# Kernel optimization log

Hardware: AMD Instinct MI355X
Metric: run time of the kernel (lower is better)

The kernel has to match this reference:

```python
import math
import jax, jax.numpy as jnp
import numpy as np

FACTOR = 5


def setup_inputs() -> dict:
    key = jax.random.key(0)
    kq, kk, kv, ki = jax.random.split(key, 4)
    B, H, L, D = 4, 8, 2048, 64
    sample_k = min(FACTOR * math.ceil(math.log(L)), L)  # 40
    queries = jax.random.normal(kq, (B, H, L, D), dtype=jnp.float32)
    keys = jax.random.normal(kk, (B, H, L, D), dtype=jnp.float32)
    values = jax.random.normal(kv, (B, H, L, D), dtype=jnp.float32)
    index_sample = jax.random.randint(ki, (L, sample_k), 0, L, dtype=jnp.int64 if jax.config.jax_enable_x64 else jnp.int32)
    return {"queries": queries, "keys": keys, "values": values, "index_sample": index_sample}


def reference(queries, keys, values, index_sample):
    B, H, L_Q, D = queries.shape
    L_K = keys.shape[2]
    u = min(FACTOR * math.ceil(math.log(L_Q)), L_Q)  # n_top queries (= 40)
    scale = 1.0 / math.sqrt(D)

    # --- _prob_QK: sparsity measurement over randomly sampled keys ---
    # K_sample[b,h,q,s,:] = keys[b,h,index_sample[q,s],:]  -> [B,H,L_Q,S,D]
    K_sample = keys[:, :, index_sample, :]
    Q_K_sample = jnp.einsum('bhqd,bhqsd->bhqs', queries, K_sample)  # [B,H,L_Q,S]
    M = Q_K_sample.max(axis=-1) - Q_K_sample.sum(axis=-1) / L_K      # [B,H,L_Q]
    _, M_top = jax.lax.top_k(M, u)                                    # [B,H,u]

    Q_reduce = jnp.take_along_axis(queries, M_top[..., None], axis=2)  # [B,H,u,D]
    scores_top = jnp.einsum('bhud,bhkd->bhuk', Q_reduce, keys) * scale  # [B,H,u,L_K]

    # --- initial context: causal cumulative sum of V (mask_flag=True) ---
    context = jnp.cumsum(values, axis=2)  # [B,H,L_Q,D]

    # --- ProbMask: causal rows gathered at the selected query indices ---
    causal = jnp.triu(jnp.ones((L_Q, L_K), dtype=bool), 1)  # [L_Q,L_K]
    mask = causal[M_top]                                     # [B,H,u,L_K]
    scores_top = jnp.where(mask, -jnp.inf, scores_top)

    attn = jax.nn.softmax(scores_top, axis=-1)                       # [B,H,u,L_K]
    update = jnp.einsum('bhuk,bhkd->bhud', attn, values)             # [B,H,u,D]

    b_idx = jnp.arange(B)[:, None, None]
    h_idx = jnp.arange(H)[None, :, None]
    context = context.at[b_idx, h_idx, M_top].set(update.astype(context.dtype))
    return context
```

## Files before the change

kernel.cpp:

```cpp
#include <hip/hip_runtime.h>
#include <math.h>

#define BB 4
#define HH 8
#define LL 2048
#define DD 64
#define SK 40
#define BH (BB*HH)
#define TILE 256
#define NTILE (LL/TILE)

__device__ __forceinline__ unsigned ordu(float v) {
    unsigned u = __float_as_uint(v);
    return (u & 0x80000000u) ? ~u : (u | 0x80000000u);
}

__global__ __launch_bounds__(256) void compute_M_kernel(
        const float* __restrict__ Q, const float* __restrict__ K,
        const int* __restrict__ IDX, float* __restrict__ M) {
    int x = blockIdx.x;
    int bhLo = x & 7;
    int r = x >> 3;
    int bhHi = r & 3;
    int chunk = r >> 2;
    int bh = bhHi * 8 + bhLo;
    int qbase = chunk * 64;
    int tid = threadIdx.x;
    int w = tid >> 6, lane = tid & 63;
    int qw = lane >> 2, c = lane & 3;
    int qi = w * 16 + qw;
    int qpos = qbase + qi;

    __shared__ int sidx[64 * SK];
    for (int i = tid; i < 64 * SK; i += 256) sidx[i] = IDX[(size_t)qbase * SK + i];

    const float4* Q4 = (const float4*)Q;
    const float4* K4 = (const float4*)K;
    float4 qreg[4];
    #pragma unroll
    for (int j = 0; j < 4; ++j)
        qreg[j] = Q4[((size_t)bh * LL + qpos) * 16 + j * 4 + c];
    __syncthreads();

    size_t kb4 = (size_t)bh * LL * 16;
    float mx = -INFINITY, sm = 0.f;
    #pragma unroll 8
    for (int s = 0; s < SK; ++s) {
        int ks = sidx[qi * SK + s];
        const float4* kr = K4 + kb4 + (size_t)ks * 16;
        float p = 0.f;
        #pragma unroll
        for (int j = 0; j < 4; ++j) {
            float4 kv = kr[j * 4 + c];
            p += qreg[j].x * kv.x + qreg[j].y * kv.y + qreg[j].z * kv.z + qreg[j].w * kv.w;
        }
        p += __shfl_xor(p, 1, 64);
        p += __shfl_xor(p, 2, 64);
        mx = fmaxf(mx, p);
        sm += p;
    }
    if (c == 0) M[(size_t)bh * LL + qpos] = mx - sm * (1.0f / (float)LL);
}

__global__ __launch_bounds__(1024) void topk_kernel(const float* __restrict__ M,
                                                    int* __restrict__ topk) {
    int bh = blockIdx.x;
    int tid = threadIdx.x;
    __shared__ unsigned hist[256];
    __shared__ unsigned bc_prefix, bc_need;
    __shared__ unsigned cnt_gt, cnt_eq;
    __shared__ int eqlist[128];

    unsigned v0 = ordu(M[(size_t)bh * LL + tid]);
    unsigned v1 = ordu(M[(size_t)bh * LL + tid + 1024]);

    unsigned prefix = 0, need = SK;
    #pragma unroll
    for (int pass = 0; pass < 4; ++pass) {
        const int s = 24 - 8 * pass;
        const unsigned maskHigh = (pass == 0) ? 0u : (0xFFFFFFFFu << (s + 8));
        if (tid < 256) hist[tid] = 0;
        __syncthreads();
        if (((v0 ^ prefix) & maskHigh) == 0) atomicAdd(&hist[(v0 >> s) & 0xFF], 1u);
        if (((v1 ^ prefix) & maskHigh) == 0) atomicAdd(&hist[(v1 >> s) & 0xFF], 1u);
        __syncthreads();
        if (tid < 256) {
            unsigned above = 0;
            for (int b = tid + 1; b < 256; ++b) above += hist[b];
            if (above < need && above + hist[tid] >= need) {
                bc_prefix = prefix | ((unsigned)tid << s);
                bc_need = need - above;
            }
        }
        __syncthreads();
        prefix = bc_prefix;
        need = bc_need;
        __syncthreads();
    }
    unsigned T = prefix;
    if (tid == 0) { cnt_gt = 0; cnt_eq = 0; }
    __syncthreads();
    if (v0 > T) { unsigned p = atomicAdd(&cnt_gt, 1u); topk[bh * SK + p] = tid; }
    else if (v0 == T) { unsigned p = atomicAdd(&cnt_eq, 1u); if (p < 128) eqlist[p] = tid; }
    if (v1 > T) { unsigned p = atomicAdd(&cnt_gt, 1u); topk[bh * SK + p] = tid + 1024; }
    else if (v1 == T) { unsigned p = atomicAdd(&cnt_eq, 1u); if (p < 128) eqlist[p] = tid + 1024; }
    __syncthreads();
    if (tid == 0) {
        int ne = (int)min(cnt_eq, 128u);
        unsigned base = cnt_gt;
        for (unsigned r2 = 0; r2 < need; ++r2) {
            int bj = 0, bv = 0x7FFFFFFF;
            for (int j = 0; j < ne; ++j)
                if (eqlist[j] < bv) { bv = eqlist[j]; bj = j; }
            topk[bh * SK + base + r2] = bv;
            eqlist[bj] = 0x7FFFFFFF;
        }
    }
}

__global__ __launch_bounds__(256) void vsum_kernel(const float* __restrict__ V,
                                                   float* __restrict__ csum) {
    int x = blockIdx.x;
    int bhLo = x & 7, r = x >> 3;
    int bhHi = r & 3, c = r >> 2;
    int bh = bhHi * 8 + bhLo;
    int tid = threadIdx.x;
    int d = tid & 63, sg = tid >> 6;
    size_t base = (size_t)bh * LL * DD;
    int row0 = c * 128 + sg * 32;
    float s = 0.f;
    for (int j = 0; j < 32; ++j) s += V[base + (size_t)(row0 + j) * DD + d];
    __shared__ float part[4][DD];
    part[sg][d] = s;
    __syncthreads();
    if (sg == 0)
        csum[((size_t)bh * 16 + c) * DD + d] = part[0][d] + part[1][d] + part[2][d] + part[3][d];
}

__global__ __launch_bounds__(256) void cumsum_kernel(const float* __restrict__ V,
                                                     const float* __restrict__ csum,
                                                     float* __restrict__ out) {
    int x = blockIdx.x;
    int bhLo = x & 7, r = x >> 3;
    int bhHi = r & 3, c = r >> 2;
    int bh = bhHi * 8 + bhLo;
    int tid = threadIdx.x;
    int d = tid & 63, sg = tid >> 6;
    size_t base = (size_t)bh * LL * DD;
    int row0 = c * 128 + sg * 32;
    float v[32];
    #pragma unroll
    for (int j = 0; j < 32; ++j) v[j] = V[base + (size_t)(row0 + j) * DD + d];
    float s = 0.f;
    #pragma unroll
    for (int j = 0; j < 32; ++j) s += v[j];
    __shared__ float part[4][DD];
    part[sg][d] = s;
    __syncthreads();
    float pre = 0.f;
    for (int cc = 0; cc < c; ++cc) pre += csum[((size_t)bh * 16 + cc) * DD + d];
    for (int ss = 0; ss < sg; ++ss) pre += part[ss][d];
    float acc = pre;
    #pragma unroll
    for (int j = 0; j < 32; ++j) {
        acc += v[j];
        out[base + (size_t)(row0 + j) * DD + d] = acc;
    }
}

__global__ __launch_bounds__(256) void attn_part_kernel(
        const float* __restrict__ Q, const float* __restrict__ K,
        const float* __restrict__ V, const int* __restrict__ topk,
        float* __restrict__ ml, float* __restrict__ ov) {
    int x = blockIdx.x;
    int bhLo = x & 7;
    int r = x >> 3;
    int u = r % SK;
    int y = r / SK;
    int bhHi = y & 3;
    int tile = y >> 2;
    int bh = bhHi * 8 + bhLo;
    int tid = threadIdx.x;

    int qpos = topk[bh * SK + u];
    int kstart = tile * TILE;
    if (kstart > qpos) return;
    int nk = min(TILE, qpos + 1 - kstart);

    const float4* Q4 = (const float4*)Q;
    const float4* K4 = (const float4*)K;
    const float4* V4 = (const float4*)V;

    int w = tid >> 6, lane = tid & 63;
    int kw = lane >> 2, c = lane & 3;
    float4 qreg[4];
    #pragma unroll
    for (int j = 0; j < 4; ++j)
        qreg[j] = Q4[((size_t)bh * LL + qpos) * 16 + j * 4 + c];

    __shared__ float se[TILE];
    __shared__ float red[4], red2[4];
    __shared__ float opart[16][16][4];

    size_t kb4 = ((size_t)bh * LL + kstart) * 16;
    #pragma unroll
    for (int rr = 0; rr < 4; ++rr) {
        int key = w * 64 + rr * 16 + kw;
        const float4* kr = K4 + kb4 + (size_t)key * 16;
        float p = 0.f;
        #pragma unroll
        for (int j = 0; j < 4; ++j) {
            float4 kv = kr[j * 4 + c];
            p += qreg[j].x * kv.x + qreg[j].y * kv.y + qreg[j].z * kv.z + qreg[j].w * kv.w;
        }
        p += __shfl_xor(p, 1, 64);
        p += __shfl_xor(p, 2, 64);
        if (c == 0) se[key] = (key < nk) ? p * 0.125f : -INFINITY;
    }
    __syncthreads();

    float sc = se[tid];
    float wv = sc;
    #pragma unroll
    for (int off = 32; off > 0; off >>= 1) wv = fmaxf(wv, __shfl_xor(wv, off, 64));
    if (lane == 0) red[w] = wv;
    __syncthreads();
    float m = fmaxf(fmaxf(red[0], red[1]), fmaxf(red[2], red[3]));
    float e = expf(sc - m);
    se[tid] = e;
    float ws = e;
    #pragma unroll
    for (int off = 32; off > 0; off >>= 1) ws += __shfl_xor(ws, off, 64);
    if (lane == 0) red2[w] = ws;
    __syncthreads();

    int slot = (bh * SK + u) * NTILE + tile;
    if (tid == 0) {
        ml[(size_t)slot * 2]     = m;
        ml[(size_t)slot * 2 + 1] = red2[0] + red2[1] + red2[2] + red2[3];
    }

    int col4 = tid & 15, kg = tid >> 4;
    float ax = 0.f, ay = 0.f, az = 0.f, aw = 0.f;
    #pragma unroll 4
    for (int j = kg; j < nk; j += 16) {
        float sj = se[j];
        float4 vv = V4[((size_t)bh * LL + kstart + j) * 16 + col4];
        ax += sj * vv.x; ay += sj * vv.y; az += sj * vv.z; aw += sj * vv.w;
    }
    opart[kg][col4][0] = ax;
    opart[kg][col4][1] = ay;
    opart[kg][col4][2] = az;
    opart[kg][col4][3] = aw;
    __syncthreads();
    if (tid < DD) {
        int c4 = tid >> 2, cp = tid & 3;
        float s = 0.f;
        #pragma unroll
        for (int kg2 = 0; kg2 < 16; ++kg2) s += opart[kg2][c4][cp];
        ov[(size_t)slot * DD + tid] = s;
    }
}

__global__ __launch_bounds__(64) void attn_combine_kernel(
        const int* __restrict__ topk, const float* __restrict__ ml,
        const float* __restrict__ ov, float* __restrict__ out) {
    int bh = blockIdx.x / SK;
    int u  = blockIdx.x % SK;
    int d = threadIdx.x;
    int qpos = topk[bh * SK + u];
    int ntile = (qpos >> 8) + 1;
    int slot0 = (bh * SK + u) * NTILE;
    float gm = -INFINITY;
    for (int t = 0; t < ntile; ++t) gm = fmaxf(gm, ml[(size_t)(slot0 + t) * 2]);
    float o = 0.f, l = 0.f;
    for (int t = 0; t < ntile; ++t) {
        float wgt = expf(ml[(size_t)(slot0 + t) * 2] - gm);
        l += ml[(size_t)(slot0 + t) * 2 + 1] * wgt;
        o += ov[(size_t)(slot0 + t) * DD + d] * wgt;
    }
    out[(size_t)bh * LL * DD + (size_t)qpos * DD + d] = o / l;
}

extern "C" void kernel_launch(void* const* d_in, const int* in_sizes, int n_in,
                              void* d_out, int out_size, void* d_ws, size_t ws_size,
                              hipStream_t stream) {
    const float* Q   = (const float*)d_in[0];
    const float* K   = (const float*)d_in[1];
    const float* V   = (const float*)d_in[2];
    const int*   IDX = (const int*)d_in[3];
    float* out = (float*)d_out;

    char* ws = (char*)d_ws;
    float* M    = (float*)ws;  ws += (size_t)BH * LL * sizeof(float);
    int*   topk = (int*)ws;    ws += ((size_t)BH * SK * sizeof(int) + 255) & ~255ull;
    float* csum = (float*)ws;  ws += (size_t)BH * 16 * DD * sizeof(float);
    float* ml   = (float*)ws;  ws += (size_t)BH * SK * NTILE * 2 * sizeof(float);
    float* ov   = (float*)ws;

    compute_M_kernel<<<1024, 256, 0, stream>>>(Q, K, IDX, M);
    topk_kernel<<<BH, 1024, 0, stream>>>(M, topk);
    vsum_kernel<<<512, 256, 0, stream>>>(V, csum);
    cumsum_kernel<<<512, 256, 0, stream>>>(V, csum, out);
    attn_part_kernel<<<BH * SK * NTILE, 256, 0, stream>>>(Q, K, V, topk, ml, ov);
    attn_combine_kernel<<<BH * SK, 64, 0, stream>>>(topk, ml, ov, out);
}
```

Before: 167.8 us.

## Merge six launches into three and drop split-K attention combine

Folds the M computation and the V chunk-sum into one launch, and the cumsum and top-k selection into another (top-k now uses 256 threads with 8 values each). The attention step now processes the whole causal key range per selected query in a single block, using a 2048-entry shared score buffer, so the partial/combine kernels and their workspace go away. This removes launch overhead and intermediate traffic, but each attention block now walks up to 2048 keys serially, which can leave the GPU underfilled with only 1280 blocks of uneven length.

```diff
diff --git a/kernel.cpp b/kernel.cpp
--- a/kernel.cpp
+++ b/kernel.cpp
@@ -7,185 +7,181 @@
 #define DD 64
 #define SK 40
 #define BH (BB*HH)
-#define TILE 256
-#define NTILE (LL/TILE)
 
 __device__ __forceinline__ unsigned ordu(float v) {
     unsigned u = __float_as_uint(v);
     return (u & 0x80000000u) ? ~u : (u | 0x80000000u);
 }
 
-__global__ __launch_bounds__(256) void compute_M_kernel(
+__global__ __launch_bounds__(256) void stage1_kernel(
         const float* __restrict__ Q, const float* __restrict__ K,
-        const int* __restrict__ IDX, float* __restrict__ M) {
-    int x = blockIdx.x;
-    int bhLo = x & 7;
-    int r = x >> 3;
-    int bhHi = r & 3;
-    int chunk = r >> 2;
-    int bh = bhHi * 8 + bhLo;
-    int qbase = chunk * 64;
+        const float* __restrict__ V, const int* __restrict__ IDX,
+        float* __restrict__ M, float* __restrict__ csum) {
     int tid = threadIdx.x;
-    int w = tid >> 6, lane = tid & 63;
-    int qw = lane >> 2, c = lane & 3;
-    int qi = w * 16 + qw;
-    int qpos = qbase + qi;
-
-    __shared__ int sidx[64 * SK];
-    for (int i = tid; i < 64 * SK; i += 256) sidx[i] = IDX[(size_t)qbase * SK + i];
-
-    const float4* Q4 = (const float4*)Q;
-    const float4* K4 = (const float4*)K;
-    float4 qreg[4];
-    #pragma unroll
-    for (int j = 0; j < 4; ++j)
-        qreg[j] = Q4[((size_t)bh * LL + qpos) * 16 + j * 4 + c];
-    __syncthreads();
-
-    size_t kb4 = (size_t)bh * LL * 16;
-    float mx = -INFINITY, sm = 0.f;
-    #pragma unroll 8
-    for (int s = 0; s < SK; ++s) {
-        int ks = sidx[qi * SK + s];
-        const float4* kr = K4 + kb4 + (size_t)ks * 16;
-        float p = 0.f;
-        #pragma unroll
-        for (int j = 0; j < 4; ++j) {
-            float4 kv = kr[j * 4 + c];
-            p += qreg[j].x * kv.x + qreg[j].y * kv.y + qreg[j].z * kv.z + qreg[j].w * kv.w;
-        }
-        p += __shfl_xor(p, 1, 64);
-        p += __shfl_xor(p, 2, 64);
-        mx = fmaxf(mx, p);
-        sm += p;
-    }
-    if (c == 0) M[(size_t)bh * LL + qpos] = mx - sm * (1.0f / (float)LL);
-}
-
-__global__ __launch_bounds__(1024) void topk_kernel(const float* __restrict__ M,
-                                                    int* __restrict__ topk) {
-    int bh = blockIdx.x;
+    if (blockIdx.x < 1024) {
+        int x = blockIdx.x;
+        int bhLo = x & 7;
+        int r = x >> 3;
+        int bhHi = r & 3;
+        int chunk = r >> 2;
+        int bh = bhHi * 8 + bhLo;
+        int qbase = chunk * 64;
+        int w = tid >> 6, lane = tid & 63;
+        int qw = lane >> 2, c = lane & 3;
+        int qi = w * 16 + qw;
+        int qpos = qbase + qi;
+
+        __shared__ int sidx[64 * SK];
+        for (int i = tid; i < 64 * SK; i += 256) sidx[i] = IDX[(size_t)qbase * SK + i];
+
+        const float4* Q4 = (const float4*)Q;
+        const float4* K4 = (const float4*)K;
+        float4 qreg[4];
+        #pragma unroll
+        for (int j = 0; j < 4; ++j)
+            qreg[j] = Q4[((size_t)bh * LL + qpos) * 16 + j * 4 + c];
+        __syncthreads();
+
+        size_t kb4 = (size_t)bh * LL * 16;
+        float mx = -INFINITY, sm = 0.f;
+        #pragma unroll 8
+        for (int s = 0; s < SK; ++s) {
+            int ks = sidx[qi * SK + s];
+            const float4* kr = K4 + kb4 + (size_t)ks * 16;
+            float p = 0.f;
+            #pragma unroll
+            for (int j = 0; j < 4; ++j) {
+                float4 kv = kr[j * 4 + c];
+                p += qreg[j].x * kv.x + qreg[j].y * kv.y + qreg[j].z * kv.z + qreg[j].w * kv.w;
+            }
+            p += __shfl_xor(p, 1, 64);
+            p += __shfl_xor(p, 2, 64);
+            mx = fmaxf(mx, p);
+            sm += p;
+        }
+        if (c == 0) M[(size_t)bh * LL + qpos] = mx - sm * (1.0f / (float)LL);
+    } else {
+        int x = blockIdx.x - 1024;
+        int bhLo = x & 7, r = x >> 3;
+        int bhHi = r & 3, c = r >> 2;
+        int bh = bhHi * 8 + bhLo;
+        int d = tid & 63, sg = tid >> 6;
+        size_t base = (size_t)bh * LL * DD;
+        int row0 = c * 128 + sg * 32;
+        float s = 0.f;
+        for (int j = 0; j < 32; ++j) s += V[base + (size_t)(row0 + j) * DD + d];
+        __shared__ float part[4][DD];
+        part[sg][d] = s;
+        __syncthreads();
+        if (sg == 0)
+            csum[((size_t)bh * 16 + c) * DD + d] = part[0][d] + part[1][d] + part[2][d] + part[3][d];
+    }
+}
+
+__global__ __launch_bounds__(256) void stage2_kernel(
+        const float* __restrict__ V, const float* __restrict__ csum,
+        const float* __restrict__ M, float* __restrict__ out,
+        int* __restrict__ topk) {
     int tid = threadIdx.x;
-    __shared__ unsigned hist[256];
-    __shared__ unsigned bc_prefix, bc_need;
-    __shared__ unsigned cnt_gt, cnt_eq;
-    __shared__ int eqlist[128];
-
-    unsigned v0 = ordu(M[(size_t)bh * LL + tid]);
-    unsigned v1 = ordu(M[(size_t)bh * LL + tid + 1024]);
-
-    unsigned prefix = 0, need = SK;
-    #pragma unroll
-    for (int pass = 0; pass < 4; ++pass) {
-        const int s = 24 - 8 * pass;
-        const unsigned maskHigh = (pass == 0) ? 0u : (0xFFFFFFFFu << (s + 8));
-        if (tid < 256) hist[tid] = 0;
-        __syncthreads();
-        if (((v0 ^ prefix) & maskHigh) == 0) atomicAdd(&hist[(v0 >> s) & 0xFF], 1u);
-        if (((v1 ^ prefix) & maskHigh) == 0) atomicAdd(&hist[(v1 >> s) & 0xFF], 1u);
-        __syncthreads();
-        if (tid < 256) {
+    if (blockIdx.x < 512) {
+        int x = blockIdx.x;
+        int bhLo = x & 7, r = x >> 3;
+        int bhHi = r & 3, c = r >> 2;
+        int bh = bhHi * 8 + bhLo;
+        int d = tid & 63, sg = tid >> 6;
+        size_t base = (size_t)bh * LL * DD;
+        int row0 = c * 128 + sg * 32;
+        float v[32];
+        #pragma unroll
+        for (int j = 0; j < 32; ++j) v[j] = V[base + (size_t)(row0 + j) * DD + d];
+        float s = 0.f;
+        #pragma unroll
+        for (int j = 0; j < 32; ++j) s += v[j];
+        __shared__ float part[4][DD];
+        part[sg][d] = s;
+        __syncthreads();
+        float pre = 0.f;
+        for (int cc = 0; cc < c; ++cc) pre += csum[((size_t)bh * 16 + cc) * DD + d];
+        for (int ss = 0; ss < sg; ++ss) pre += part[ss][d];
+        float acc = pre;
+        #pragma unroll
+        for (int j = 0; j < 32; ++j) {
+            acc += v[j];
+            out[base + (size_t)(row0 + j) * DD + d] = acc;
+        }
+    } else {
+        int bh = blockIdx.x - 512;
+        __shared__ unsigned hist[256];
+        __shared__ unsigned bc_prefix, bc_need;
+        __shared__ unsigned cnt_gt, cnt_eq;
+        __shared__ int eqlist[128];
+
+        unsigned v[8];
+        #pragma unroll
+        for (int j = 0; j < 8; ++j)
+            v[j] = ordu(M[(size_t)bh * LL + tid + j * 256]);
+
+        unsigned prefix = 0, need = SK;
+        #pragma unroll
+        for (int pass = 0; pass < 4; ++pass) {
+            const int s = 24 - 8 * pass;
+            const unsigned maskHigh = (pass == 0) ? 0u : (0xFFFFFFFFu << (s + 8));
+            hist[tid] = 0;
+            __syncthreads();
+            #pragma unroll
+            for (int j = 0; j < 8; ++j)
+                if (((v[j] ^ prefix) & maskHigh) == 0)
+                    atomicAdd(&hist[(v[j] >> s) & 0xFF], 1u);
+            __syncthreads();
             unsigned above = 0;
             for (int b = tid + 1; b < 256; ++b) above += hist[b];
             if (above < need && above + hist[tid] >= need) {
                 bc_prefix = prefix | ((unsigned)tid << s);
                 bc_need = need - above;
             }
-        }
-        __syncthreads();
-        prefix = bc_prefix;
-        need = bc_need;
-        __syncthreads();
-    }
-    unsigned T = prefix;
-    if (tid == 0) { cnt_gt = 0; cnt_eq = 0; }
-    __syncthreads();
-    if (v0 > T) { unsigned p = atomicAdd(&cnt_gt, 1u); topk[bh * SK + p] = tid; }
-    else if (v0 == T) { unsigned p = atomicAdd(&cnt_eq, 1u); if (p < 128) eqlist[p] = tid; }
-    if (v1 > T) { unsigned p = atomicAdd(&cnt_gt, 1u); topk[bh * SK + p] = tid + 1024; }
-    else if (v1 == T) { unsigned p = atomicAdd(&cnt_eq, 1u); if (p < 128) eqlist[p] = tid + 1024; }
-    __syncthreads();
-    if (tid == 0) {
-        int ne = (int)min(cnt_eq, 128u);
-        unsigned base = cnt_gt;
-        for (unsigned r2 = 0; r2 < need; ++r2) {
-            int bj = 0, bv = 0x7FFFFFFF;
-            for (int j = 0; j < ne; ++j)
-                if (eqlist[j] < bv) { bv = eqlist[j]; bj = j; }
-            topk[bh * SK + base + r2] = bv;
-            eqlist[bj] = 0x7FFFFFFF;
-        }
-    }
-}
-
-__global__ __launch_bounds__(256) void vsum_kernel(const float* __restrict__ V,
-                                                   float* __restrict__ csum) {
+            __syncthreads();
+            prefix = bc_prefix;
+            need = bc_need;
+            __syncthreads();
+        }
+        unsigned T = prefix;
+        if (tid == 0) { cnt_gt = 0; cnt_eq = 0; }
+        __syncthreads();
+        #pragma unroll
+        for (int j = 0; j < 8; ++j) {
+            int idx = tid + j * 256;
+            if (v[j] > T) { unsigned p = atomicAdd(&cnt_gt, 1u); topk[bh * SK + p] = idx; }
+            else if (v[j] == T) { unsigned p = atomicAdd(&cnt_eq, 1u); if (p < 128) eqlist[p] = idx; }
+        }
+        __syncthreads();
+        if (tid == 0) {
+            int ne = (int)min(cnt_eq, 128u);
+            unsigned base = cnt_gt;
+            for (unsigned r2 = 0; r2 < need; ++r2) {
+                int bj = 0, bv = 0x7FFFFFFF;
+                for (int j = 0; j < ne; ++j)
+                    if (eqlist[j] < bv) { bv = eqlist[j]; bj = j; }
+                topk[bh * SK + base + r2] = bv;
+                eqlist[bj] = 0x7FFFFFFF;
+            }
+        }
+    }
+}
+
+__global__ __launch_bounds__(256) void attn_kernel(
+        const float* __restrict__ Q, const float* __restrict__ K,
+        const float* __restrict__ V, const int* __restrict__ topk,
+        float* __restrict__ out) {
     int x = blockIdx.x;
-    int bhLo = x & 7, r = x >> 3;
-    int bhHi = r & 3, c = r >> 2;
+    int bhLo = x & 7;
+    int t = x >> 3;
+    int u = t % SK;
+    int bhHi = t / SK;
     int bh = bhHi * 8 + bhLo;
     int tid = threadIdx.x;
-    int d = tid & 63, sg = tid >> 6;
-    size_t base = (size_t)bh * LL * DD;
-    int row0 = c * 128 + sg * 32;
-    float s = 0.f;
-    for (int j = 0; j < 32; ++j) s += V[base + (size_t)(row0 + j) * DD + d];
-    __shared__ float part[4][DD];
-    part[sg][d] = s;
-    __syncthreads();
-    if (sg == 0)
-        csum[((size_t)bh * 16 + c) * DD + d] = part[0][d] + part[1][d] + part[2][d] + part[3][d];
-}
-
-__global__ __launch_bounds__(256) void cumsum_kernel(const float* __restrict__ V,
-                                                     const float* __restrict__ csum,
-                                                     float* __restrict__ out) {
-    int x = blockIdx.x;
-    int bhLo = x & 7, r = x >> 3;
-    int bhHi = r & 3, c = r >> 2;
-    int bh = bhHi * 8 + bhLo;
-    int tid = threadIdx.x;
-    int d = tid & 63, sg = tid >> 6;
-    size_t base = (size_t)bh * LL * DD;
-    int row0 = c * 128 + sg * 32;
-    float v[32];
-    #pragma unroll
-    for (int j = 0; j < 32; ++j) v[j] = V[base + (size_t)(row0 + j) * DD + d];
-    float s = 0.f;
-    #pragma unroll
-    for (int j = 0; j < 32; ++j) s += v[j];
-    __shared__ float part[4][DD];
-    part[sg][d] = s;
-    __syncthreads();
-    float pre = 0.f;
-    for (int cc = 0; cc < c; ++cc) pre += csum[((size_t)bh * 16 + cc) * DD + d];
-    for (int ss = 0; ss < sg; ++ss) pre += part[ss][d];
-    float acc = pre;
-    #pragma unroll
-    for (int j = 0; j < 32; ++j) {
-        acc += v[j];
-        out[base + (size_t)(row0 + j) * DD + d] = acc;
-    }
-}
-
-__global__ __launch_bounds__(256) void attn_part_kernel(
-        const float* __restrict__ Q, const float* __restrict__ K,
-        const float* __restrict__ V, const int* __restrict__ topk,
-        float* __restrict__ ml, float* __restrict__ ov) {
-    int x = blockIdx.x;
-    int bhLo = x & 7;
-    int r = x >> 3;
-    int u = r % SK;
-    int y = r / SK;
-    int bhHi = y & 3;
-    int tile = y >> 2;
-    int bh = bhHi * 8 + bhLo;
-    int tid = threadIdx.x;
 
     int qpos = topk[bh * SK + u];
-    int kstart = tile * TILE;
-    if (kstart > qpos) return;
-    int nk = min(TILE, qpos + 1 - kstart);
+    int nk = qpos + 1;
 
     const float4* Q4 = (const float4*)Q;
     const float4* K4 = (const float4*)K;
@@ -198,54 +194,54 @@
     for (int j = 0; j < 4; ++j)
         qreg[j] = Q4[((size_t)bh * LL + qpos) * 16 + j * 4 + c];
 
-    __shared__ float se[TILE];
+    __shared__ float sc[LL];
     __shared__ float red[4], red2[4];
     __shared__ float opart[16][16][4];
 
-    size_t kb4 = ((size_t)bh * LL + kstart) * 16;
+    size_t kb4 = (size_t)bh * LL * 16;
+    int rounds = (nk + 63) >> 6;
+    for (int rr = 0; rr < rounds; ++rr) {
+        int key = rr * 64 + w * 16 + kw;
+        if (key < nk) {
+            const float4* kr = K4 + kb4 + (size_t)key * 16;
+            float p = 0.f;
+            #pragma unroll
+            for (int j = 0; j < 4; ++j) {
+                float4 kv = kr[j * 4 + c];
+                p += qreg[j].x * kv.x + qreg[j].y * kv.y + qreg[j].z * kv.z + qreg[j].w * kv.w;
+            }
+            p += __shfl_xor(p, 1, 64);
+            p += __shfl_xor(p, 2, 64);
+            if (c == 0) sc[key] = p * 0.125f;
+        }
+    }
+    __syncthreads();
+
+    float m = -INFINITY;
+    for (int j = tid; j < nk; j += 256) m = fmaxf(m, sc[j]);
     #pragma unroll
-    for (int rr = 0; rr < 4; ++rr) {
-        int key = w * 64 + rr * 16 + kw;
-        const float4* kr = K4 + kb4 + (size_t)key * 16;
-        float p = 0.f;
-        #pragma unroll
-        for (int j = 0; j < 4; ++j) {
-            float4 kv = kr[j * 4 + c];
-            p += qreg[j].x * kv.x + qreg[j].y * kv.y + qreg[j].z * kv.z + qreg[j].w * kv.w;
-        }
-        p += __shfl_xor(p, 1, 64);
-        p += __shfl_xor(p, 2, 64);
-        if (c == 0) se[key] = (key < nk) ? p * 0.125f : -INFINITY;
-    }
-    __syncthreads();
-
-    float sc = se[tid];
-    float wv = sc;
+    for (int off = 32; off > 0; off >>= 1) m = fmaxf(m, __shfl_xor(m, off, 64));
+    if (lane == 0) red[w] = m;
+    __syncthreads();
+    m = fmaxf(fmaxf(red[0], red[1]), fmaxf(red[2], red[3]));
+
+    float ls = 0.f;
+    for (int j = tid; j < nk; j += 256) {
+        float e = expf(sc[j] - m);
+        sc[j] = e;
+        ls += e;
+    }
     #pragma unroll
-    for (int off = 32; off > 0; off >>= 1) wv = fmaxf(wv, __shfl_xor(wv, off, 64));
-    if (lane == 0) red[w] = wv;
-    __syncthreads();
-    float m = fmaxf(fmaxf(red[0], red[1]), fmaxf(red[2], red[3]));
-    float e = expf(sc - m);
-    se[tid] = e;
-    float ws = e;
-    #pragma unroll
-    for (int off = 32; off > 0; off >>= 1) ws += __shfl_xor(ws, off, 64);
-    if (lane == 0) red2[w] = ws;
-    __syncthreads();
-
-    int slot = (bh * SK + u) * NTILE + tile;
-    if (tid == 0) {
-        ml[(size_t)slot * 2]     = m;
-        ml[(size_t)slot * 2 + 1] = red2[0] + red2[1] + red2[2] + red2[3];
-    }
+    for (int off = 32; off > 0; off >>= 1) ls += __shfl_xor(ls, off, 64);
+    if (lane == 0) red2[w] = ls;
+    __syncthreads();
+    float linv = 1.0f / (red2[0] + red2[1] + red2[2] + red2[3]);
 
     int col4 = tid & 15, kg = tid >> 4;
     float ax = 0.f, ay = 0.f, az = 0.f, aw = 0.f;
-    #pragma unroll 4
     for (int j = kg; j < nk; j += 16) {
-        float sj = se[j];
-        float4 vv = V4[((size_t)bh * LL + kstart + j) * 16 + col4];
+        float sj = sc[j];
+        float4 vv = V4[((size_t)bh * LL + j) * 16 + col4];
         ax += sj * vv.x; ay += sj * vv.y; az += sj * vv.z; aw += sj * vv.w;
     }
     opart[kg][col4][0] = ax;
@@ -258,28 +254,8 @@
         float s = 0.f;
         #pragma unroll
         for (int kg2 = 0; kg2 < 16; ++kg2) s += opart[kg2][c4][cp];
-        ov[(size_t)slot * DD + tid] = s;
-    }
-}
-
-__global__ __launch_bounds__(64) void attn_combine_kernel(
-        const int* __restrict__ topk, const float* __restrict__ ml,
-        const float* __restrict__ ov, float* __restrict__ out) {
-    int bh = blockIdx.x / SK;
-    int u  = blockIdx.x % SK;
-    int d = threadIdx.x;
-    int qpos = topk[bh * SK + u];
-    int ntile = (qpos >> 8) + 1;
-    int slot0 = (bh * SK + u) * NTILE;
-    float gm = -INFINITY;
-    for (int t = 0; t < ntile; ++t) gm = fmaxf(gm, ml[(size_t)(slot0 + t) * 2]);
-    float o = 0.f, l = 0.f;
-    for (int t = 0; t < ntile; ++t) {
-        float wgt = expf(ml[(size_t)(slot0 + t) * 2] - gm);
-        l += ml[(size_t)(slot0 + t) * 2 + 1] * wgt;
-        o += ov[(size_t)(slot0 + t) * DD + d] * wgt;
-    }
-    out[(size_t)bh * LL * DD + (size_t)qpos * DD + d] = o / l;
+        out[((size_t)bh * LL + qpos) * DD + tid] = s * linv;
+    }
 }
 
 extern "C" void kernel_launch(void* const* d_in, const int* in_sizes, int n_in,
@@ -294,14 +270,9 @@
     char* ws = (char*)d_ws;
     float* M    = (float*)ws;  ws += (size_t)BH * LL * sizeof(float);
     int*   topk = (int*)ws;    ws += ((size_t)BH * SK * sizeof(int) + 255) & ~255ull;
-    float* csum = (float*)ws;  ws += (size_t)BH * 16 * DD * sizeof(float);
-    float* ml   = (float*)ws;  ws += (size_t)BH * SK * NTILE * 2 * sizeof(float);
-    float* ov   = (float*)ws;
-
-    compute_M_kernel<<<1024, 256, 0, stream>>>(Q, K, IDX, M);
-    topk_kernel<<<BH, 1024, 0, stream>>>(M, topk);
-    vsum_kernel<<<512, 256, 0, stream>>>(V, csum);
-    cumsum_kernel<<<512, 256, 0, stream>>>(V, csum, out);
-    attn_part_kernel<<<BH * SK * NTILE, 256, 0, stream>>>(Q, K, V, topk, ml, ov);
-    attn_combine_kernel<<<BH * SK, 64, 0, stream>>>(topk, ml, ov, out);
-}
+    float* csum = (float*)ws;
+
+    stage1_kernel<<<1536, 256, 0, stream>>>(Q, K, V, IDX, M, csum);
+    stage2_kernel<<<544, 256, 0, stream>>>(V, csum, M, out, topk);
+    attn_kernel<<<BH * SK, 256, 0, stream>>>(Q, K, V, topk, out);
+}
```

After: 166.5 us. Within noise of the previous version (-0.8%).
